# Kernel tuning notes

Measured on AMD Instinct MI355X. Metric: run time of the kernel, lower is better.

The kernel has to match this reference:

```python
import jax, jax.numpy as jnp
import numpy as np

KS = 3          # kernel_size
M = 6           # num_bases
TEM = 6         # tem_size = (KS//2)*num_bases
BN_EPS = 1e-3   # keras BatchNormalization default epsilon


def _conv(x, w):
    # x: NCHW, w: OIHW, stride 1, SAME padding (module uses padding='same')
    return jax.lax.conv_general_dilated(x, w, (1, 1), 'SAME',
                                        dimension_numbers=('NCHW', 'OIHW', 'NCHW'))


def _bn(x, gamma, beta, mean, var):
    # inference-mode batchnorm over channel dim (NCHW)
    s = gamma * jax.lax.rsqrt(var + BN_EPS)
    return x * s[None, :, None, None] + (beta - mean * s)[None, :, None, None]


def _unfold(x):
    # im2col: N,C,H,W -> N,C,KS*KS,H,W with SAME padding, stride 1
    N, C, H, W = x.shape
    xp = jnp.pad(x, ((0, 0), (0, 0), (1, 1), (1, 1)))
    taps = [xp[:, :, i:i + H, j:j + W] for i in range(KS) for j in range(KS)]
    return jnp.stack(taps, axis=2)


def setup_inputs() -> dict:
    key = jax.random.key(0)
    ks = jax.random.split(key, 16)
    N, C, O, H, W = 16, 128, 128, 64, 64
    inter, bsz = 64, M * TEM  # 64, 36
    x = jax.random.normal(ks[0], (N, C, H, W), jnp.float32)
    w1 = jax.random.normal(ks[1], (inter, C, 3, 3), jnp.float32) * (1.0 / np.sqrt(C * 9))
    gamma1 = jnp.ones((inter,), jnp.float32)
    beta1 = jnp.zeros((inter,), jnp.float32)
    mean1 = jax.random.normal(ks[2], (inter,), jnp.float32) * 0.1
    var1 = jax.random.uniform(ks[3], (inter,), jnp.float32, 0.5, 1.5)
    w2 = jax.random.normal(ks[4], (bsz, inter, 3, 3), jnp.float32) * (1.0 / np.sqrt(inter * 9))
    gamma2 = jnp.ones((bsz,), jnp.float32)
    beta2 = jnp.zeros((bsz,), jnp.float32)
    mean2 = jax.random.normal(ks[5], (bsz,), jnp.float32) * 0.1
    var2 = jax.random.uniform(ks[6], (bsz,), jnp.float32, 0.5, 1.5)
    # Fixed Fourier-Bessel-style basis [TEM, KS*KS], normalized as in calculate_FB_bases
    rng = np.random.RandomState(0)
    psi = rng.normal(size=(KS * KS, TEM)).astype(np.float32)
    c = np.sqrt((psi ** 2).sum(0).mean())
    fb_bases = jnp.asarray((psi / c).T)  # [TEM, 9]
    coef = jax.random.normal(ks[7], (O, C * M), jnp.float32) * np.sqrt(2.0 / (C * M))
    bias = jnp.zeros((O,), jnp.float32)
    return {'x': x, 'w1': w1, 'gamma1': gamma1, 'beta1': beta1, 'mean1': mean1,
            'var1': var1, 'w2': w2, 'gamma2': gamma2, 'beta2': beta2,
            'mean2': mean2, 'var2': var2, 'fb_bases': fb_bases, 'coef': coef,
            'bias': bias}


def reference(x, w1, gamma1, beta1, mean1, var1, w2, gamma2, beta2, mean2, var2,
              fb_bases, coef, bias):
    N, C, H, W = x.shape
    # bases_net: conv3x3 -> BN -> tanh -> conv3x3 -> BN -> tanh
    h = jnp.tanh(_bn(_conv(x, w1), gamma1, beta1, mean1, var1))
    b = jnp.tanh(_bn(_conv(h, w2), gamma2, beta2, mean2, var2))   # N,36,H,W
    bcoef = b.reshape(N, M, TEM, H, W)
    # combine predicted coefficients with fixed FB bases -> per-pixel filters
    bases = jnp.einsum('bmkhw,kl->bmlhw', bcoef, fb_bases)        # N,M,9,H,W
    xu = _unfold(x)                                               # N,C,9,H,W
    # per-pixel gather-multiply-reduce over the 9 taps
    bo = jnp.einsum('bmlhw,bclhw->bcmhw', bases, xu)              # N,C,M,H,W
    bo = bo.reshape(N, C * M, H, W)
    # 1x1 conv with coef + bias
    out = jnp.einsum('bkhw,ok->bohw', bo, coef) + bias[None, :, None, None]
    return out
```

## Files before the change

### kernel.cpp

```cpp
#include <hip/hip_runtime.h>
#include <hip/hip_bf16.h>

using bf16 = __hip_bfloat16;
typedef __attribute__((ext_vector_type(8))) short bf16x8;
typedef __attribute__((ext_vector_type(4))) float f32x4;
typedef __attribute__((ext_vector_type(2))) float f32x2;

#define BN_EPS 1e-3f

#define OFF_FLAG  0u
#define OFF_W1M   16u
#define OFF_B1F   36880u
#define OFF_W2M   36944u
#define OFF_B2F   50768u
#define OFF_FBF   50804u
#define OFF_CFM   50860u
#define OFF_BIASF 100012u
#define OFF_BB    100144u

__device__ __forceinline__ float b2f(bf16 v) { return __bfloat162float(v); }
__device__ __forceinline__ unsigned short f2b(float f) {
    union { bf16 h; unsigned short u; } cv;
    cv.h = __float2bfloat16(f);
    return cv.u;
}
__device__ __forceinline__ unsigned packbf(float a, float b) {
    return (unsigned)f2b(a) | ((unsigned)f2b(b) << 16);
}
__device__ __forceinline__ float ldin(const void* p, long long i, int f) {
    return f ? b2f(((const bf16*)p)[i]) : ((const float*)p)[i];
}
__device__ __forceinline__ float lo_f(unsigned u) { return __uint_as_float(u << 16); }
__device__ __forceinline__ float hi_f(unsigned u) { return __uint_as_float(u & 0xFFFF0000u); }
__device__ __forceinline__ void ld8f(const void* p, long long i, int f, float* o) {
    if (f) {
        uint4 v = *(const uint4*)((const unsigned short*)p + i);
        o[0] = lo_f(v.x); o[1] = hi_f(v.x); o[2] = lo_f(v.y); o[3] = hi_f(v.y);
        o[4] = lo_f(v.z); o[5] = hi_f(v.z); o[6] = lo_f(v.w); o[7] = hi_f(v.w);
    } else {
        const float* q = (const float*)p + i;
        float4 a = *(const float4*)q, b = *(const float4*)(q + 4);
        o[0] = a.x; o[1] = a.y; o[2] = a.z; o[3] = a.w;
        o[4] = b.x; o[5] = b.y; o[6] = b.z; o[7] = b.w;
    }
}
__device__ __forceinline__ bf16x8 lds_frag(const unsigned short* p) {
    uint2 lo = *(const uint2*)p;
    uint2 hi = *(const uint2*)(p + 4);
    union { unsigned u[4]; bf16x8 v; } r;
    r.u[0] = lo.x; r.u[1] = lo.y; r.u[2] = hi.x; r.u[3] = hi.y;
    return r.v;
}

__global__ void detect_kernel(const void* __restrict__ g1, float* __restrict__ ws) {
    if (threadIdx.x == 0) {
        unsigned w = ((const unsigned*)g1)[0];
        ws[OFF_FLAG] = (w == 0x3F800000u) ? 0.f : 1.f;
    }
}

__global__ __launch_bounds__(256) void prep_kernel(
    const void* __restrict__ w1, const void* __restrict__ g1, const void* __restrict__ be1,
    const void* __restrict__ mu1, const void* __restrict__ va1,
    const void* __restrict__ w2, const void* __restrict__ g2, const void* __restrict__ be2,
    const void* __restrict__ mu2, const void* __restrict__ va2,
    const void* __restrict__ fb, const void* __restrict__ coef, const void* __restrict__ bias,
    float* __restrict__ ws)
{
    const int f = (ws[OFF_FLAG] != 0.f);
    int j = blockIdx.x * 256 + threadIdx.x;
    if (j < 73728) {
        int tap = j >> 13, r = j & 8191;
        int ntile = r >> 11, r2 = r & 2047;
        int ks = r2 >> 9, r3 = r2 & 511;
        int lane = r3 >> 3, jj = r3 & 7;
        int oc = ntile * 16 + (lane & 15);
        int ic = ks * 32 + (lane >> 4) * 8 + jj;
        float s = ldin(g1, oc, f) * rsqrtf(ldin(va1, oc, f) + BN_EPS);
        ((unsigned short*)(ws + OFF_W1M))[j] = f2b(ldin(w1, (oc * 128 + ic) * 9 + tap, f) * s);
        return;
    }
    j -= 73728;
    if (j < 64) {
        float s = ldin(g1, j, f) * rsqrtf(ldin(va1, j, f) + BN_EPS);
        ws[OFF_B1F + j] = ldin(be1, j, f) - ldin(mu1, j, f) * s;
        return;
    }
    j -= 64;
    if (j < 27648) {
        int tap = j / 3072, r = j - tap * 3072;
        int ntile = r >> 10, r2 = r & 1023;
        int ks = r2 >> 9, r3 = r2 & 511;
        int lane = r3 >> 3, jj = r3 & 7;
        int oc = ntile * 16 + (lane & 15);
        int ic = ks * 32 + (lane >> 4) * 8 + jj;
        float v = 0.f;
        if (oc < 36) {
            float s = ldin(g2, oc, f) * rsqrtf(ldin(va2, oc, f) + BN_EPS);
            v = ldin(w2, (oc * 64 + ic) * 9 + tap, f) * s;
        }
        ((unsigned short*)(ws + OFF_W2M))[j] = f2b(v);
        return;
    }
    j -= 27648;
    if (j < 36) {
        float s = ldin(g2, j, f) * rsqrtf(ldin(va2, j, f) + BN_EPS);
        ws[OFF_B2F + j] = ldin(be2, j, f) - ldin(mu2, j, f) * s;
        return;
    }
    j -= 36;
    if (j < 54) { ws[OFF_FBF + j] = ldin(fb, j, f); return; }
    j -= 54;
    if (j < 98304) {
        int chunk = j / 12288, r = j - chunk * 12288;
        int ks = r >> 12, r2 = r & 4095;
        int ntile = r2 >> 9, r3 = r2 & 511;
        int lane = r3 >> 3, jj = r3 & 7;
        int o = ntile * 16 + (lane & 15);
        int k = chunk * 96 + ks * 32 + (lane >> 4) * 8 + jj;
        ((unsigned short*)(ws + OFF_CFM))[j] = f2b(ldin(coef, o * 768 + k, f));
        return;
    }
    j -= 98304;
    if (j < 128) { ws[OFF_BIASF + j] = ldin(bias, j, f); return; }
}

__global__ __launch_bounds__(256) void conv1_mfma(
    const void* __restrict__ x, const float* __restrict__ ws,
    unsigned short* __restrict__ hbuf)
{
    __shared__ unsigned short sA[3][66][132];
    unsigned* sAu = (unsigned*)sA;
    const unsigned short* w1m = (const unsigned short*)(ws + OFF_W1M);
    const int f = (ws[OFF_FLAG] != 0.f);
    const int t = threadIdx.x;
    const int n = blockIdx.x >> 6, h = blockIdx.x & 63;

    for (int e = t; e < 396; e += 256) {
        int dy = e / 132, q = e - dy * 132;
        int wrow = (q >= 66) ? 65 : 0;
        int cu = (q >= 66) ? q - 66 : q;
        sAu[(dy * 66 + wrow) * 66 + cu] = 0u;
    }
    {
        const long long xb = (long long)n * 128 * 4096;
        for (int u = t; u < 1536; u += 256) {
            int dy = u >> 9, rem = u & 511, icp = rem >> 3, w8 = rem & 7;
            int hh = h + dy - 1;
            float va[8], vb[8];
            if (hh >= 0 && hh < 64) {
                long long base = xb + (long long)(icp * 2) * 4096 + hh * 64 + w8 * 8;
                ld8f(x, base, f, va);
                ld8f(x, base + 4096, f, vb);
            } else {
#pragma unroll
                for (int i = 0; i < 8; ++i) { va[i] = 0.f; vb[i] = 0.f; }
            }
            const int wb_ = w8 * 8 + 1;
#pragma unroll
            for (int i = 0; i < 8; ++i)
                sAu[(dy * 66 + wb_ + i) * 66 + icp] = packbf(va[i], vb[i]);
        }
    }
    __syncthreads();

    const int wv = t >> 6, lane = t & 63;
    const int fr = lane & 15, quad = lane >> 4;
    const int mh = (wv & 1) * 32, nh = (wv >> 1) * 32;
    const int ntb = nh >> 4;

    f32x4 acc[2][2];
#pragma unroll
    for (int i = 0; i < 2; ++i)
#pragma unroll
        for (int j = 0; j < 2; ++j) acc[i][j] = (f32x4){0.f, 0.f, 0.f, 0.f};

#pragma unroll
    for (int tap = 0; tap < 9; ++tap) {
        const int dy = tap / 3, dx = tap - dy * 3;
#pragma unroll
        for (int ks = 0; ks < 4; ++ks) {
            const int kof = ks * 32 + quad * 8;
            bf16x8 a0 = lds_frag(&sA[dy][mh + fr + dx][kof]);
            bf16x8 a1 = lds_frag(&sA[dy][mh + 16 + fr + dx][kof]);
            bf16x8 b0 = *(const bf16x8*)(w1m + (((tap * 4 + ntb) * 4 + ks) * 64 + lane) * 8);
            bf16x8 b1 = *(const bf16x8*)(w1m + (((tap * 4 + ntb + 1) * 4 + ks) * 64 + lane) * 8);
            acc[0][0] = __builtin_amdgcn_mfma_f32_16x16x32_bf16(a0, b0, acc[0][0], 0, 0, 0);
            acc[0][1] = __builtin_amdgcn_mfma_f32_16x16x32_bf16(a0, b1, acc[0][1], 0, 0, 0);
            acc[1][0] = __builtin_amdgcn_mfma_f32_16x16x32_bf16(a1, b0, acc[1][0], 0, 0, 0);
            acc[1][1] = __builtin_amdgcn_mfma_f32_16x16x32_bf16(a1, b1, acc[1][1], 0, 0, 0);
        }
    }

#pragma unroll
    for (int mt = 0; mt < 2; ++mt)
#pragma unroll
        for (int nt = 0; nt < 2; ++nt) {
            int oc = nh + nt * 16 + fr;
            int m0 = mh + mt * 16 + quad * 4;
            float bv = ws[OFF_B1F + oc];
            f32x4 v = acc[mt][nt];
            union { unsigned short us[4]; uint2 u; } pk;
#pragma unroll
            for (int i = 0; i < 4; ++i) pk.us[i] = f2b(tanhf(v[i] + bv));
            *(uint2*)(hbuf + (size_t)(n * 64 + oc) * 4096 + h * 64 + m0) = pk.u;
        }
}

__global__ __launch_bounds__(256) void conv2_mfma(
    const float* __restrict__ ws, const unsigned short* __restrict__ hbuf,
    float* __restrict__ bbout)
{
    __shared__ unsigned short sA[3][66][68];
    unsigned* sAu = (unsigned*)sA;
    const unsigned short* w2m = (const unsigned short*)(ws + OFF_W2M);
    const int t = threadIdx.x;
    const int n = blockIdx.x >> 6, h = blockIdx.x & 63;

    for (int e = t; e < 204; e += 256) {
        int dy = e / 68, q = e - dy * 68;
        int wrow = (q >= 34) ? 65 : 0;
        int cu = (q >= 34) ? q - 34 : q;
        sAu[(dy * 66 + wrow) * 34 + cu] = 0u;
    }
    {
        const unsigned short* hn = hbuf + (size_t)n * 64 * 4096;
        for (int u = t; u < 768; u += 256) {
            int dy = u >> 8, rem = u & 255, icp = rem >> 3, w8 = rem & 7;
            int hh = h + dy - 1;
            uint4 a = make_uint4(0u, 0u, 0u, 0u), b = a;
            if (hh >= 0 && hh < 64) {
                const unsigned short* p = hn + (size_t)(icp * 2) * 4096 + hh * 64 + w8 * 8;
                a = *(const uint4*)p;
                b = *(const uint4*)(p + 4096);
            }
            const int wb_ = w8 * 8 + 1;
            unsigned au[4] = {a.x, a.y, a.z, a.w}, bu[4] = {b.x, b.y, b.z, b.w};
#pragma unroll
            for (int jj = 0; jj < 4; ++jj) {
                unsigned lo = (au[jj] & 0xFFFFu) | (bu[jj] << 16);
                unsigned hi = (au[jj] >> 16) | (bu[jj] & 0xFFFF0000u);
                sAu[(dy * 66 + wb_ + 2 * jj) * 34 + icp] = lo;
                sAu[(dy * 66 + wb_ + 2 * jj + 1) * 34 + icp] = hi;
            }
        }
    }
    __syncthreads();

    const int wv = t >> 6, lane = t & 63;
    const int fr = lane & 15, quad = lane >> 4;
    const int m0 = wv * 16;

    f32x4 acc[3];
#pragma unroll
    for (int i = 0; i < 3; ++i) acc[i] = (f32x4){0.f, 0.f, 0.f, 0.f};

#pragma unroll
    for (int tap = 0; tap < 9; ++tap) {
        const int dy = tap / 3, dx = tap - dy * 3;
#pragma unroll
        for (int ks = 0; ks < 2; ++ks) {
            const int kof = ks * 32 + quad * 8;
            bf16x8 a = lds_frag(&sA[dy][m0 + fr + dx][kof]);
#pragma unroll
            for (int nt = 0; nt < 3; ++nt) {
                bf16x8 b = *(const bf16x8*)(w2m + (((tap * 3 + nt) * 2 + ks) * 64 + lane) * 8);
                acc[nt] = __builtin_amdgcn_mfma_f32_16x16x32_bf16(a, b, acc[nt], 0, 0, 0);
            }
        }
    }

    const int pbase = (n << 12) + h * 64 + m0 + quad * 4;
#pragma unroll
    for (int nt = 0; nt < 3; ++nt) {
        int oc = nt * 16 + fr;
        if (oc < 36) {
            float bv = ws[OFF_B2F + oc];
            f32x4 v = acc[nt];
#pragma unroll
            for (int reg = 0; reg < 4; ++reg)
                bbout[(size_t)(pbase + reg) * 36 + oc] = tanhf(v[reg] + bv);
        }
    }
}

__global__ __launch_bounds__(512) void fuse_kernel(
    const void* __restrict__ x, const float* __restrict__ ws, void* __restrict__ outv)
{
    __shared__ float sbT[64][60];
    __shared__ __align__(16) unsigned short slbo[64][104];
    __shared__ __align__(16) unsigned short sX[3][66][20];
    unsigned* sXu = (unsigned*)sX;

    const float* bbp = ws + OFF_BB;
    const float* fbf = ws + OFF_FBF;
    const unsigned short* cfm = (const unsigned short*)(ws + OFF_CFM);
    const int f = (ws[OFF_FLAG] != 0.f);

    const int t = threadIdx.x;
    const int p0 = blockIdx.x * 64;
    const int n = p0 >> 12;
    const int h = (p0 >> 6) & 63;

    for (int task = t; task < 64 * 54; task += 512) {
        int p = task & 63, j = task >> 6;
        int m = j / 9, l = j - m * 9;
        const float* br = bbp + (size_t)(p0 + p) * 36 + m * 6;
        float s = 0.f;
#pragma unroll
        for (int k = 0; k < 6; ++k) s += br[k] * fbf[k * 9 + l];
        sbT[p][l * 6 + m] = s;
    }
    if (t < 48) {
        int dy = t >> 4, q = t & 15;
        int wrow = (q >= 8) ? 65 : 0;
        sXu[(dy * 66 + wrow) * 10 + (q & 7)] = 0u;
    }

    const int pp = t >> 3, cl = t & 7;
    const int wv = t >> 6, lane = t & 63;
    const int fr = lane & 15, quad = lane >> 4;
    const int m0w = (wv & 3) * 16;
    const int nh = (wv >> 2) * 64;
    const int ntb = nh >> 4;

    f32x4 acc[4];
#pragma unroll
    for (int nt = 0; nt < 4; ++nt) acc[nt] = (f32x4){0.f, 0.f, 0.f, 0.f};

    const long long xbase = (long long)n * 128 * 4096;
    const int sw = t & 63, sg = t >> 6;

    for (int c0 = 0; c0 < 128; c0 += 16) {
        const int chunk = c0 >> 4;
#pragma unroll
        for (int u = sg; u < 24; u += 8) {
            int dy = u >> 3, icp = u & 7;
            int hh = h + dy - 1;
            float v0 = 0.f, v1 = 0.f;
            if (hh >= 0 && hh < 64) {
                long long base = xbase + (long long)(c0 + icp * 2) * 4096 + hh * 64 + sw;
                v0 = ldin(x, base, f);
                v1 = ldin(x, base + 4096, f);
            }
            sXu[(dy * 66 + sw + 1) * 10 + icp] = packbf(v0, v1);
        }
        __syncthreads();
        {
            f32x2 xv[9];
#pragma unroll
            for (int dy = 0; dy < 3; ++dy)
#pragma unroll
                for (int dx = 0; dx < 3; ++dx) {
                    unsigned d = sXu[(dy * 66 + pp + dx) * 10 + cl];
                    xv[dy * 3 + dx] = (f32x2){lo_f(d), hi_f(d)};
                }
            f32x2 sm2[6];
#pragma unroll
            for (int m = 0; m < 6; ++m) sm2[m] = (f32x2){0.f, 0.f};
            const float* sp = &sbT[pp][0];
#pragma unroll
            for (int jv = 0; jv < 13; ++jv) {
                f32x4 s4 = *(const f32x4*)(sp + jv * 4);
#pragma unroll
                for (int e = 0; e < 4; ++e) {
                    const int j = jv * 4 + e;
                    const int l = j / 6, m = j - l * 6;
                    sm2[m] += xv[l] * s4[e];
                }
            }
            {
                f32x2 s2 = *(const f32x2*)(sp + 52);
                sm2[4] += xv[8] * s2[0];
                sm2[5] += xv[8] * s2[1];
            }
            unsigned* du = (unsigned*)slbo + pp * 52 + cl * 6;
            uint2 w0 = make_uint2(packbf(sm2[0][0], sm2[1][0]), packbf(sm2[2][0], sm2[3][0]));
            uint2 w1 = make_uint2(packbf(sm2[4][0], sm2[5][0]), packbf(sm2[0][1], sm2[1][1]));
            uint2 w2 = make_uint2(packbf(sm2[2][1], sm2[3][1]), packbf(sm2[4][1], sm2[5][1]));
            *(uint2*)&du[0] = w0;
            *(uint2*)&du[2] = w1;
            *(uint2*)&du[4] = w2;
        }
        __syncthreads();
#pragma unroll
        for (int ks = 0; ks < 3; ++ks) {
            const int kof = ks * 32 + quad * 8;
            bf16x8 a = *(const bf16x8*)&slbo[m0w + fr][kof];
            const unsigned short* cb = cfm + ((chunk * 3 + ks) * 8 + ntb) * 512 + lane * 8;
            bf16x8 b0 = *(const bf16x8*)(cb);
            bf16x8 b1 = *(const bf16x8*)(cb + 512);
            bf16x8 b2 = *(const bf16x8*)(cb + 1024);
            bf16x8 b3 = *(const bf16x8*)(cb + 1536);
            acc[0] = __builtin_amdgcn_mfma_f32_16x16x32_bf16(a, b0, acc[0], 0, 0, 0);
            acc[1] = __builtin_amdgcn_mfma_f32_16x16x32_bf16(a, b1, acc[1], 0, 0, 0);
            acc[2] = __builtin_amdgcn_mfma_f32_16x16x32_bf16(a, b2, acc[2], 0, 0, 0);
            acc[3] = __builtin_amdgcn_mfma_f32_16x16x32_bf16(a, b3, acc[3], 0, 0, 0);
        }
    }

    const int mrow = m0w + quad * 4;
#pragma unroll
    for (int nt = 0; nt < 4; ++nt) {
        int o = nh + nt * 16 + fr;
        float bv = ws[OFF_BIASF + o];
        f32x4 v = acc[nt];
        size_t ofs = (size_t)(n * 128 + o) * 4096 + h * 64 + mrow;
        if (f) {
            union { unsigned short us[4]; uint2 u; } pk;
#pragma unroll
            for (int i = 0; i < 4; ++i) pk.us[i] = f2b(v[i] + bv);
            *(uint2*)((unsigned short*)outv + ofs) = pk.u;
        } else {
            float4 w4 = make_float4(v[0] + bv, v[1] + bv, v[2] + bv, v[3] + bv);
            *(float4*)((float*)outv + ofs) = w4;
        }
    }
}

extern "C" void kernel_launch(void* const* d_in, const int* in_sizes, int n_in,
                              void* d_out, int out_size, void* d_ws, size_t ws_size,
                              hipStream_t stream)
{
    float* ws = (float*)d_ws;
    unsigned short* hbuf = (unsigned short*)d_out;

    hipLaunchKernelGGL(detect_kernel, dim3(1), dim3(64), 0, stream, d_in[2], ws);
    hipLaunchKernelGGL(prep_kernel, dim3(782), dim3(256), 0, stream,
                       d_in[1], d_in[2], d_in[3], d_in[4], d_in[5],
                       d_in[6], d_in[7], d_in[8], d_in[9], d_in[10],
                       d_in[11], d_in[12], d_in[13], ws);
    hipLaunchKernelGGL(conv1_mfma, dim3(1024), dim3(256), 0, stream, d_in[0], ws, hbuf);
    hipLaunchKernelGGL(conv2_mfma, dim3(1024), dim3(256), 0, stream, ws, hbuf, ws + OFF_BB);
    hipLaunchKernelGGL(fuse_kernel, dim3(1024), dim3(512), 0, stream, d_in[0], ws, d_out);
}
```

Before: 214.3 us.

## Double block size for conv kernels and prefetch x chunks into registers in fuse

conv1 and conv2 now launch 512 threads per block, with 8 waves splitting the output tile so each wave does fewer MFMAs. This is meant to give more waves per CU to hide LDS and global latency. The fuse kernel now loads the next 16-channel chunk of x into registers while the current chunk is being computed, overlapping global loads with compute. Launch bounds of (512,8) are added, which can force register caps and spills. conv2's split is unbalanced (waves 4-7 do 1 tile versus 2 for waves 0-3) and introduces a wave-uniform branch.

```diff
diff --git a/kernel.cpp b/kernel.cpp
--- a/kernel.cpp
+++ b/kernel.cpp
@@ -125,7 +125,7 @@
     if (j < 128) { ws[OFF_BIASF + j] = ldin(bias, j, f); return; }
 }
 
-__global__ __launch_bounds__(256) void conv1_mfma(
+__global__ __launch_bounds__(512, 8) void conv1_mfma(
     const void* __restrict__ x, const float* __restrict__ ws,
     unsigned short* __restrict__ hbuf)
 {
@@ -136,7 +136,7 @@
     const int t = threadIdx.x;
     const int n = blockIdx.x >> 6, h = blockIdx.x & 63;
 
-    for (int e = t; e < 396; e += 256) {
+    for (int e = t; e < 396; e += 512) {
         int dy = e / 132, q = e - dy * 132;
         int wrow = (q >= 66) ? 65 : 0;
         int cu = (q >= 66) ? q - 66 : q;
@@ -144,7 +144,7 @@
     }
     {
         const long long xb = (long long)n * 128 * 4096;
-        for (int u = t; u < 1536; u += 256) {
+        for (int u = t; u < 1536; u += 512) {
             int dy = u >> 9, rem = u & 511, icp = rem >> 3, w8 = rem & 7;
             int hh = h + dy - 1;
             float va[8], vb[8];
@@ -166,14 +166,13 @@
 
     const int wv = t >> 6, lane = t & 63;
     const int fr = lane & 15, quad = lane >> 4;
-    const int mh = (wv & 1) * 32, nh = (wv >> 1) * 32;
+    const int mh = (wv & 3) * 16;
+    const int nh = (wv >> 2) * 32;
     const int ntb = nh >> 4;
 
-    f32x4 acc[2][2];
-#pragma unroll
-    for (int i = 0; i < 2; ++i)
-#pragma unroll
-        for (int j = 0; j < 2; ++j) acc[i][j] = (f32x4){0.f, 0.f, 0.f, 0.f};
+    f32x4 acc[2];
+#pragma unroll
+    for (int j = 0; j < 2; ++j) acc[j] = (f32x4){0.f, 0.f, 0.f, 0.f};
 
 #pragma unroll
     for (int tap = 0; tap < 9; ++tap) {
@@ -181,33 +180,28 @@
 #pragma unroll
         for (int ks = 0; ks < 4; ++ks) {
             const int kof = ks * 32 + quad * 8;
-            bf16x8 a0 = lds_frag(&sA[dy][mh + fr + dx][kof]);
-            bf16x8 a1 = lds_frag(&sA[dy][mh + 16 + fr + dx][kof]);
+            bf16x8 a = lds_frag(&sA[dy][mh + fr + dx][kof]);
             bf16x8 b0 = *(const bf16x8*)(w1m + (((tap * 4 + ntb) * 4 + ks) * 64 + lane) * 8);
             bf16x8 b1 = *(const bf16x8*)(w1m + (((tap * 4 + ntb + 1) * 4 + ks) * 64 + lane) * 8);
-            acc[0][0] = __builtin_amdgcn_mfma_f32_16x16x32_bf16(a0, b0, acc[0][0], 0, 0, 0);
-            acc[0][1] = __builtin_amdgcn_mfma_f32_16x16x32_bf16(a0, b1, acc[0][1], 0, 0, 0);
-            acc[1][0] = __builtin_amdgcn_mfma_f32_16x16x32_bf16(a1, b0, acc[1][0], 0, 0, 0);
-            acc[1][1] = __builtin_amdgcn_mfma_f32_16x16x32_bf16(a1, b1, acc[1][1], 0, 0, 0);
-        }
-    }
-
-#pragma unroll
-    for (int mt = 0; mt < 2; ++mt)
-#pragma unroll
-        for (int nt = 0; nt < 2; ++nt) {
-            int oc = nh + nt * 16 + fr;
-            int m0 = mh + mt * 16 + quad * 4;
-            float bv = ws[OFF_B1F + oc];
-            f32x4 v = acc[mt][nt];
-            union { unsigned short us[4]; uint2 u; } pk;
-#pragma unroll
-            for (int i = 0; i < 4; ++i) pk.us[i] = f2b(tanhf(v[i] + bv));
-            *(uint2*)(hbuf + (size_t)(n * 64 + oc) * 4096 + h * 64 + m0) = pk.u;
-        }
-}
-
-__global__ __launch_bounds__(256) void conv2_mfma(
+            acc[0] = __builtin_amdgcn_mfma_f32_16x16x32_bf16(a, b0, acc[0], 0, 0, 0);
+            acc[1] = __builtin_amdgcn_mfma_f32_16x16x32_bf16(a, b1, acc[1], 0, 0, 0);
+        }
+    }
+
+#pragma unroll
+    for (int nt = 0; nt < 2; ++nt) {
+        int oc = nh + nt * 16 + fr;
+        int m0 = mh + quad * 4;
+        float bv = ws[OFF_B1F + oc];
+        f32x4 v = acc[nt];
+        union { unsigned short us[4]; uint2 u; } pk;
+#pragma unroll
+        for (int i = 0; i < 4; ++i) pk.us[i] = f2b(tanhf(v[i] + bv));
+        *(uint2*)(hbuf + (size_t)(n * 64 + oc) * 4096 + h * 64 + m0) = pk.u;
+    }
+}
+
+__global__ __launch_bounds__(512, 8) void conv2_mfma(
     const float* __restrict__ ws, const unsigned short* __restrict__ hbuf,
     float* __restrict__ bbout)
 {
@@ -217,7 +211,7 @@
     const int t = threadIdx.x;
     const int n = blockIdx.x >> 6, h = blockIdx.x & 63;
 
-    for (int e = t; e < 204; e += 256) {
+    for (int e = t; e < 204; e += 512) {
         int dy = e / 68, q = e - dy * 68;
         int wrow = (q >= 34) ? 65 : 0;
         int cu = (q >= 34) ? q - 34 : q;
@@ -225,7 +219,7 @@
     }
     {
         const unsigned short* hn = hbuf + (size_t)n * 64 * 4096;
-        for (int u = t; u < 768; u += 256) {
+        for (int u = t; u < 768; u += 512) {
             int dy = u >> 8, rem = u & 255, icp = rem >> 3, w8 = rem & 7;
             int hh = h + dy - 1;
             uint4 a = make_uint4(0u, 0u, 0u, 0u), b = a;
@@ -249,11 +243,12 @@
 
     const int wv = t >> 6, lane = t & 63;
     const int fr = lane & 15, quad = lane >> 4;
-    const int m0 = wv * 16;
-
-    f32x4 acc[3];
-#pragma unroll
-    for (int i = 0; i < 3; ++i) acc[i] = (f32x4){0.f, 0.f, 0.f, 0.f};
+    const int m0 = (wv & 3) * 16;
+    const int ngrp = wv >> 2;
+
+    f32x4 acc[2];
+#pragma unroll
+    for (int i = 0; i < 2; ++i) acc[i] = (f32x4){0.f, 0.f, 0.f, 0.f};
 
 #pragma unroll
     for (int tap = 0; tap < 9; ++tap) {
@@ -262,21 +257,34 @@
         for (int ks = 0; ks < 2; ++ks) {
             const int kof = ks * 32 + quad * 8;
             bf16x8 a = lds_frag(&sA[dy][m0 + fr + dx][kof]);
-#pragma unroll
-            for (int nt = 0; nt < 3; ++nt) {
-                bf16x8 b = *(const bf16x8*)(w2m + (((tap * 3 + nt) * 2 + ks) * 64 + lane) * 8);
-                acc[nt] = __builtin_amdgcn_mfma_f32_16x16x32_bf16(a, b, acc[nt], 0, 0, 0);
+            if (ngrp == 0) {
+                bf16x8 b0 = *(const bf16x8*)(w2m + (((tap * 3 + 0) * 2 + ks) * 64 + lane) * 8);
+                bf16x8 b1 = *(const bf16x8*)(w2m + (((tap * 3 + 1) * 2 + ks) * 64 + lane) * 8);
+                acc[0] = __builtin_amdgcn_mfma_f32_16x16x32_bf16(a, b0, acc[0], 0, 0, 0);
+                acc[1] = __builtin_amdgcn_mfma_f32_16x16x32_bf16(a, b1, acc[1], 0, 0, 0);
+            } else {
+                bf16x8 b2 = *(const bf16x8*)(w2m + (((tap * 3 + 2) * 2 + ks) * 64 + lane) * 8);
+                acc[0] = __builtin_amdgcn_mfma_f32_16x16x32_bf16(a, b2, acc[0], 0, 0, 0);
             }
         }
     }
 
     const int pbase = (n << 12) + h * 64 + m0 + quad * 4;
-#pragma unroll
-    for (int nt = 0; nt < 3; ++nt) {
-        int oc = nt * 16 + fr;
+    if (ngrp == 0) {
+#pragma unroll
+        for (int nt = 0; nt < 2; ++nt) {
+            int oc = nt * 16 + fr;
+            float bv = ws[OFF_B2F + oc];
+            f32x4 v = acc[nt];
+#pragma unroll
+            for (int reg = 0; reg < 4; ++reg)
+                bbout[(size_t)(pbase + reg) * 36 + oc] = tanhf(v[reg] + bv);
+        }
+    } else {
+        int oc = 32 + fr;
         if (oc < 36) {
             float bv = ws[OFF_B2F + oc];
-            f32x4 v = acc[nt];
+            f32x4 v = acc[0];
 #pragma unroll
             for (int reg = 0; reg < 4; ++reg)
                 bbout[(size_t)(pbase + reg) * 36 + oc] = tanhf(v[reg] + bv);
@@ -284,7 +292,7 @@
     }
 }
 
-__global__ __launch_bounds__(512) void fuse_kernel(
+__global__ __launch_bounds__(512, 8) void fuse_kernel(
     const void* __restrict__ x, const float* __restrict__ ws, void* __restrict__ outv)
 {
     __shared__ float sbT[64][60];
@@ -302,6 +310,22 @@
     const int n = p0 >> 12;
     const int h = (p0 >> 6) & 63;
 
+    const long long xbase = (long long)n * 128 * 4096;
+    const int sw = t & 63, sg = t >> 6;
+
+    float rv0[3], rv1[3];
+#pragma unroll
+    for (int dy = 0; dy < 3; ++dy) {
+        int hh = h + dy - 1;
+        float v0 = 0.f, v1 = 0.f;
+        if (hh >= 0 && hh < 64) {
+            long long base = xbase + (long long)(sg * 2) * 4096 + hh * 64 + sw;
+            v0 = ldin(x, base, f);
+            v1 = ldin(x, base + 4096, f);
+        }
+        rv0[dy] = v0; rv1[dy] = v1;
+    }
+
     for (int task = t; task < 64 * 54; task += 512) {
         int p = task & 63, j = task >> 6;
         int m = j / 9, l = j - m * 9;
@@ -328,24 +352,28 @@
 #pragma unroll
     for (int nt = 0; nt < 4; ++nt) acc[nt] = (f32x4){0.f, 0.f, 0.f, 0.f};
 
-    const long long xbase = (long long)n * 128 * 4096;
-    const int sw = t & 63, sg = t >> 6;
-
-    for (int c0 = 0; c0 < 128; c0 += 16) {
-        const int chunk = c0 >> 4;
-#pragma unroll
-        for (int u = sg; u < 24; u += 8) {
-            int dy = u >> 3, icp = u & 7;
-            int hh = h + dy - 1;
-            float v0 = 0.f, v1 = 0.f;
-            if (hh >= 0 && hh < 64) {
-                long long base = xbase + (long long)(c0 + icp * 2) * 4096 + hh * 64 + sw;
-                v0 = ldin(x, base, f);
-                v1 = ldin(x, base + 4096, f);
-            }
-            sXu[(dy * 66 + sw + 1) * 10 + icp] = packbf(v0, v1);
-        }
+    __syncthreads();
+
+#pragma unroll
+    for (int chunk = 0; chunk < 8; ++chunk) {
+#pragma unroll
+        for (int dy = 0; dy < 3; ++dy)
+            sXu[(dy * 66 + sw + 1) * 10 + sg] = packbf(rv0[dy], rv1[dy]);
         __syncthreads();
+        if (chunk < 7) {
+            const int c0n = (chunk + 1) * 16;
+#pragma unroll
+            for (int dy = 0; dy < 3; ++dy) {
+                int hh = h + dy - 1;
+                float v0 = 0.f, v1 = 0.f;
+                if (hh >= 0 && hh < 64) {
+                    long long base = xbase + (long long)(c0n + sg * 2) * 4096 + hh * 64 + sw;
+                    v0 = ldin(x, base, f);
+                    v1 = ldin(x, base + 4096, f);
+                }
+                rv0[dy] = v0; rv1[dy] = v1;
+            }
+        }
         {
             f32x2 xv[9];
 #pragma unroll
@@ -430,7 +458,7 @@
                        d_in[1], d_in[2], d_in[3], d_in[4], d_in[5],
                        d_in[6], d_in[7], d_in[8], d_in[9], d_in[10],
                        d_in[11], d_in[12], d_in[13], ws);
-    hipLaunchKernelGGL(conv1_mfma, dim3(1024), dim3(256), 0, stream, d_in[0], ws, hbuf);
-    hipLaunchKernelGGL(conv2_mfma, dim3(1024), dim3(256), 0, stream, ws, hbuf, ws + OFF_BB);
+    hipLaunchKernelGGL(conv1_mfma, dim3(1024), dim3(512), 0, stream, d_in[0], ws, hbuf);
+    hipLaunchKernelGGL(conv2_mfma, dim3(1024), dim3(512), 0, stream, ws, hbuf, ws + OFF_BB);
     hipLaunchKernelGGL(fuse_kernel, dim3(1024), dim3(512), 0, stream, d_in[0], ws, d_out);
 }
```

Result: faster. 201.7 us (-5.9%).
